# Performance work log

Hardware: AMD Instinct MI355X
Metric: run time of the kernel (lower is better)

## Reference

```python
import jax, jax.numpy as jnp
import numpy as np

DIM = 768
NUM_HEADS = 12
DECAY_RATE = 5.0


def setup_inputs() -> dict:
    key = jax.random.key(0)
    k1, k2, k3, k4 = jax.random.split(key, 4)
    B, N, C = 4, 1024, DIM
    x = jax.random.normal(k1, (B, N, C), dtype=jnp.float32)
    # torch nn.Linear weights: y = x @ W.T ; qkv_bias=False
    qkv_w = jax.random.normal(k2, (3 * C, C), dtype=jnp.float32) * (1.0 / np.sqrt(C))
    proj_w = jax.random.normal(k3, (C, C), dtype=jnp.float32) * (1.0 / np.sqrt(C))
    proj_b = jax.random.normal(k4, (C,), dtype=jnp.float32) * 0.01
    return {"x": x, "qkv_w": qkv_w, "proj_w": proj_w, "proj_b": proj_b, "cur_epoch": 3}


def reference(x, qkv_w, proj_w, proj_b, cur_epoch):
    B, N, C = x.shape
    H = NUM_HEADS
    hd = C // H
    scale = hd ** -0.5

    qkv = (x @ qkv_w.T).reshape(B, N, 3, H, hd).transpose(2, 0, 3, 1, 4)  # [3,B,H,N,hd]
    q, k, v = qkv[0], qkv[1], qkv[2]

    scores = jnp.einsum("bhqd,bhkd->bhqk", q, k) * scale
    logp = jax.nn.log_softmax(scores, axis=-1)
    attn = jnp.exp(logp)  # [B,H,N,N]

    # Per-key entropy: column j of attn flattened over (B,H,N) is renormalized
    # by Categorical; dividing by num_heads cancels under normalization.
    # H(p/s) = log(s) - (1/s) * sum(p * log p)
    s = jnp.sum(attn, axis=(0, 1, 2))                 # [N]
    plogp = jnp.sum(attn * logp, axis=(0, 1, 2))      # [N]
    entropies = jnp.log(s) - plogp / s

    # threshold decay: factor = sum_{i=0}^{cur_epoch-1} decay*exp(-(i+1))
    factor = DECAY_RATE * float(np.sum(np.exp(-(np.arange(cur_epoch) + 1.0))))
    entropy_threshold = float(np.log(C)) - factor

    # attn[:,:,:,keep] @ v[:,:,keep,:] == (attn * mask) @ v  (zeroed columns drop out)
    mask = (entropies <= entropy_threshold).astype(attn.dtype)  # [N]
    out = jnp.einsum("bhqk,bhkd->bhqd", attn * mask[None, None, None, :], v)
    out = out.transpose(0, 2, 1, 3).reshape(B, N, C)
    out = out @ proj_w.T + proj_b
    return out
```

## Files before the change

kernel.cpp:

```cpp
#include <hip/hip_runtime.h>


typedef __bf16 bf16x8 __attribute__((ext_vector_type(8)));
typedef __bf16 bf16x4 __attribute__((ext_vector_type(4)));
typedef float  f32x4  __attribute__((ext_vector_type(4)));

#define MFMA16(a, b, c) __builtin_amdgcn_mfma_f32_16x16x32_bf16((a), (b), (c), 0, 0, 0)
#define LOG2E_8 0.18033688f

__global__ __launch_bounds__(256) void kc_conv(
    const float* __restrict__ x, const float* __restrict__ qw, const float* __restrict__ pw,
    __bf16* __restrict__ xb, __bf16* __restrict__ qwb, __bf16* __restrict__ pwb,
    float* __restrict__ colSP, int* __restrict__ keepCnt)
{
  const int i = blockIdx.x * 256 + threadIdx.x;
  const float4* src;
  __bf16* dst;
  int j;
  if (i < 786432)       { src = (const float4*)x;  dst = xb;  j = i; }
  else if (i < 1228800) { src = (const float4*)qw; dst = qwb; j = i - 786432; }
  else                  { src = (const float4*)pw; dst = pwb; j = i - 1228800; }
  const float4 f = src[j];
  bf16x4 o;
  o[0] = (__bf16)f.x; o[1] = (__bf16)f.y; o[2] = (__bf16)f.z; o[3] = (__bf16)f.w;
  *(bf16x4*)(dst + 4 * (size_t)j) = o;
  if (i < 2048) colSP[i] = 0.f;
  if (i == 0) *keepCnt = 0;
}

__global__ __launch_bounds__(256) void kg_qkv(
    const __bf16* __restrict__ A, const __bf16* __restrict__ Bm,
    __bf16* __restrict__ qb, __bf16* __restrict__ kb, float* __restrict__ v)
{
  __shared__ __bf16 As[2][64 * 72];
  __shared__ __bf16 Bs[2][64 * 72];
  const int tid = threadIdx.x;
  const int w = tid >> 6, lane = tid & 63, quad = lane >> 4, l = lane & 15;
  const int r0 = blockIdx.y * 64, c0 = blockIdx.x * 64;
  const int row = tid >> 3, ko = (tid & 7) * 8;
  const f32x4 zero = {0.f, 0.f, 0.f, 0.f};
  f32x4 acc[4];
#pragma unroll
  for (int ct = 0; ct < 4; ++ct) acc[ct] = zero;

  uint4 a0 = *(const uint4*)(A + (size_t)(r0 + row) * 768 + ko);
  uint4 a1 = *(const uint4*)(A + (size_t)(r0 + row + 32) * 768 + ko);
  uint4 b0 = *(const uint4*)(Bm + (size_t)(c0 + row) * 768 + ko);
  uint4 b1 = *(const uint4*)(Bm + (size_t)(c0 + row + 32) * 768 + ko);

  for (int k0 = 0; k0 < 768; k0 += 64) {
    const int buf = (k0 >> 6) & 1;
    *(uint4*)&As[buf][row * 72 + ko] = a0;
    *(uint4*)&As[buf][(row + 32) * 72 + ko] = a1;
    *(uint4*)&Bs[buf][row * 72 + ko] = b0;
    *(uint4*)&Bs[buf][(row + 32) * 72 + ko] = b1;
    __syncthreads();
    if (k0 < 704) {
      a0 = *(const uint4*)(A + (size_t)(r0 + row) * 768 + k0 + 64 + ko);
      a1 = *(const uint4*)(A + (size_t)(r0 + row + 32) * 768 + k0 + 64 + ko);
      b0 = *(const uint4*)(Bm + (size_t)(c0 + row) * 768 + k0 + 64 + ko);
      b1 = *(const uint4*)(Bm + (size_t)(c0 + row + 32) * 768 + k0 + 64 + ko);
    }
    const bf16x8 af0 = *(const bf16x8*)&As[buf][(w * 16 + l) * 72 + quad * 8];
    const bf16x8 af1 = *(const bf16x8*)&As[buf][(w * 16 + l) * 72 + 32 + quad * 8];
#pragma unroll
    for (int ct = 0; ct < 4; ++ct) {
      const bf16x8 bf0 = *(const bf16x8*)&Bs[buf][(ct * 16 + l) * 72 + quad * 8];
      const bf16x8 bf1 = *(const bf16x8*)&Bs[buf][(ct * 16 + l) * 72 + 32 + quad * 8];
      acc[ct] = MFMA16(af0, bf0, acc[ct]);
      acc[ct] = MFMA16(af1, bf1, acc[ct]);
    }
  }
  const int part = c0 / 768;
  const int h = (c0 % 768) >> 6;
#pragma unroll
  for (int ct = 0; ct < 4; ++ct) {
    const int d = ct * 16 + l;
#pragma unroll
    for (int i = 0; i < 4; ++i) {
      const int rg = r0 + w * 16 + quad * 4 + i;
      const int b_ = rg >> 10, n = rg & 1023;
      const size_t off = ((size_t)(b_ * 12 + h) * 1024 + n) * 64 + d;
      const float val = acc[ct][i];
      if (part == 0)      qb[off] = (__bf16)val;
      else if (part == 1) kb[off] = (__bf16)val;
      else                v[off]  = val;
    }
  }
}

__global__ __launch_bounds__(256) void ks_fused(
    const __bf16* __restrict__ qb, const __bf16* __restrict__ kb,
    float* __restrict__ lse, float* __restrict__ colSP)
{
  __shared__ __bf16 Ks[2][64 * 72];
  __shared__ float sS[1024];
  __shared__ float sP[1024];
  __shared__ float zrow[64];
  const int tid = threadIdx.x;
  const int w = tid >> 6, lane = tid & 63, quad = lane >> 4, l = lane & 15;
  const int bh = blockIdx.x, r0 = blockIdx.y * 64;
  const int row = tid >> 3, ko = (tid & 7) * 8;
  for (int i = tid; i < 1024; i += 256) { sS[i] = 0.f; sP[i] = 0.f; }
  if (tid < 64) zrow[tid] = 0.f;

  const __bf16* qbase = qb + ((size_t)bh * 1024 + r0 + l) * 64;
  bf16x8 aq0[4], aq1[4];
#pragma unroll
  for (int rt = 0; rt < 4; ++rt) {
    aq0[rt] = *(const bf16x8*)(qbase + rt * 1024 + quad * 8);
    aq1[rt] = *(const bf16x8*)(qbase + rt * 1024 + 32 + quad * 8);
  }
  const __bf16* kbase = kb + (size_t)bh * 65536;
  const f32x4 zero = {0.f, 0.f, 0.f, 0.f};
  const int koff = (w * 16 + l) * 72 + quad * 8;

  uint4 ka0 = *(const uint4*)(kbase + (size_t)row * 64 + ko);
  uint4 ka1 = *(const uint4*)(kbase + (size_t)(row + 32) * 64 + ko);

  float z[16] = {};
  for (int s = 0; s < 16; ++s) {
    __bf16* Kw = Ks[s & 1];
    *(uint4*)&Kw[row * 72 + ko] = ka0;
    *(uint4*)&Kw[(row + 32) * 72 + ko] = ka1;
    __syncthreads();
    const int nxt = (s + 1) & 15;
    ka0 = *(const uint4*)(kbase + (size_t)(nxt * 64 + row) * 64 + ko);
    ka1 = *(const uint4*)(kbase + (size_t)(nxt * 64 + row + 32) * 64 + ko);
    const bf16x8 kf0 = *(const bf16x8*)&Kw[koff];
    const bf16x8 kf1 = *(const bf16x8*)&Kw[koff + 32];
#pragma unroll
    for (int rt = 0; rt < 4; ++rt) {
      f32x4 acc = MFMA16(aq0[rt], kf0, zero);
      acc = MFMA16(aq1[rt], kf1, acc);
#pragma unroll
      for (int r = 0; r < 4; ++r) z[rt * 4 + r] += exp2f(acc[r] * LOG2E_8);
    }
  }
#pragma unroll
  for (int off = 1; off < 16; off <<= 1) {
#pragma unroll
    for (int i = 0; i < 16; ++i) z[i] += __shfl_xor(z[i], off);
  }
  if (l == 0) {
#pragma unroll
    for (int rt = 0; rt < 4; ++rt)
#pragma unroll
      for (int r = 0; r < 4; ++r)
        atomicAdd(&zrow[rt * 16 + quad * 4 + r], z[rt * 4 + r]);
  }
  __syncthreads();
  if (tid < 64) lse[bh * 1024 + r0 + tid] = __logf(zrow[tid]);
  float nlb[16], nlg[16];
#pragma unroll
  for (int rt = 0; rt < 4; ++rt) {
#pragma unroll
    for (int r = 0; r < 4; ++r) {
      const float Z = zrow[rt * 16 + quad * 4 + r];
      const float lg = __logf(Z);
      nlg[rt * 4 + r] = -lg;
      nlb[rt * 4 + r] = -lg * 1.44269504f;
    }
  }

  for (int s = 0; s < 16; ++s) {
    __bf16* Kw = Ks[s & 1];
    *(uint4*)&Kw[row * 72 + ko] = ka0;
    *(uint4*)&Kw[(row + 32) * 72 + ko] = ka1;
    __syncthreads();
    if (s < 15) {
      ka0 = *(const uint4*)(kbase + (size_t)((s + 1) * 64 + row) * 64 + ko);
      ka1 = *(const uint4*)(kbase + (size_t)((s + 1) * 64 + row + 32) * 64 + ko);
    }
    const bf16x8 kf0 = *(const bf16x8*)&Kw[koff];
    const bf16x8 kf1 = *(const bf16x8*)&Kw[koff + 32];
    float cs = 0.f, cp = 0.f;
#pragma unroll
    for (int rt = 0; rt < 4; ++rt) {
      f32x4 acc = MFMA16(aq0[rt], kf0, zero);
      acc = MFMA16(aq1[rt], kf1, acc);
#pragma unroll
      for (int r = 0; r < 4; ++r) {
        const float a = acc[r];
        const float t = exp2f(fmaf(a, LOG2E_8, nlb[rt * 4 + r]));
        const float d = fmaf(a, 0.125f, nlg[rt * 4 + r]);
        cs += t;
        cp = fmaf(t, d, cp);
      }
    }
    cs += __shfl_xor(cs, 16); cs += __shfl_xor(cs, 32);
    cp += __shfl_xor(cp, 16); cp += __shfl_xor(cp, 32);
    if (lane < 16) {
      sS[s * 64 + w * 16 + l] += cs;
      sP[s * 64 + w * 16 + l] += cp;
    }
  }
  __syncthreads();
  for (int i = tid; i < 1024; i += 256) {
    atomicAdd(&colSP[i], sS[i]);
    atomicAdd(&colSP[1024 + i], sP[i]);
  }
}

__global__ void k_mask(const float* __restrict__ colSP, const int* __restrict__ cur_epoch,
                       float* __restrict__ mask, int* __restrict__ keepCnt)
{
  const int j = threadIdx.x;
  const float s = colSP[j];
  const float ent = __logf(s) - colSP[1024 + j] / s;
  const int ce = cur_epoch[0];
  float factor = 0.f;
  for (int i = 1; i <= ce; ++i) factor += __expf(-(float)i);
  factor *= 5.0f;
  const float thr = __logf(768.0f) - factor;
  const int keep = (ent <= thr) ? 1 : 0;
  mask[j] = keep ? 1.0f : 0.0f;
  if (keep) atomicAdd(keepCnt, 1);
}

__global__ __launch_bounds__(256) void k_av(
    const __bf16* __restrict__ qb, const __bf16* __restrict__ kb,
    const float* __restrict__ v, const float* __restrict__ lse,
    const float* __restrict__ mask, const int* __restrict__ keepCnt,
    __bf16* __restrict__ ctxb)
{
  if (*keepCnt == 0) return;
  const int tid = threadIdx.x;
  const int bh = blockIdx.x, r0 = blockIdx.y * 32;
  const int b_ = bh / 12, h = bh % 12;
  __shared__ float qs[32][64];
  __shared__ float pbuf[4][8][64];
  for (int i = tid; i < 2048; i += 256)
    qs[i >> 6][i & 63] = (float)qb[((size_t)bh * 1024 + r0) * 64 + i];
  __syncthreads();
  const int w = tid >> 6, l = tid & 63, rb = w * 8;
  float ls[8];
#pragma unroll
  for (int i = 0; i < 8; ++i) ls[i] = lse[bh * 1024 + r0 + rb + i];
  float acc[8] = {};
  for (int chunk = 0; chunk < 16; ++chunk) {
    const float mk = mask[chunk * 64 + l];
    if (__ballot(mk != 0.0f) == 0ull) continue;
    const __bf16* kp = kb + ((size_t)bh * 1024 + chunk * 64 + l) * 64;
    float s[8] = {};
    for (int d0 = 0; d0 < 64; d0 += 8) {
      const bf16x8 kf = *(const bf16x8*)(kp + d0);
#pragma unroll
      for (int dd = 0; dd < 8; ++dd) {
        const float kv = (float)kf[dd];
#pragma unroll
        for (int i = 0; i < 8; ++i) s[i] += qs[rb + i][d0 + dd] * kv;
      }
    }
    __syncthreads();
#pragma unroll
    for (int i = 0; i < 8; ++i)
      pbuf[w][i][l] = __expf(s[i] * 0.125f - ls[i]) * mk;
    __syncthreads();
    const float* vp = v + ((size_t)bh * 1024 + chunk * 64) * 64 + l;
    for (int jj = 0; jj < 64; ++jj) {
      const float vv = vp[(size_t)jj * 64];
#pragma unroll
      for (int i = 0; i < 8; ++i) acc[i] += pbuf[w][i][jj] * vv;
    }
  }
#pragma unroll
  for (int i = 0; i < 8; ++i)
    ctxb[((size_t)(b_ * 1024 + r0 + rb + i)) * 768 + h * 64 + l] = (__bf16)acc[i];
}

__global__ __launch_bounds__(256) void kg_proj(
    const __bf16* __restrict__ A, const __bf16* __restrict__ Bm,
    const float* __restrict__ bias, const int* __restrict__ keepCnt,
    float* __restrict__ out)
{
  const int tid = threadIdx.x;
  const int w = tid >> 6, lane = tid & 63, quad = lane >> 4, l = lane & 15;
  const int r0 = blockIdx.y * 64, c0 = blockIdx.x * 64;
  if (*keepCnt == 0) {
#pragma unroll
    for (int ct = 0; ct < 4; ++ct) {
      const int c = c0 + ct * 16 + l;
      const float bv = bias[c];
#pragma unroll
      for (int i = 0; i < 4; ++i) {
        const int rg = r0 + w * 16 + quad * 4 + i;
        out[(size_t)rg * 768 + c] = bv;
      }
    }
    return;
  }
  __shared__ __bf16 As[64 * 72];
  __shared__ __bf16 Bs[64 * 72];
  const int row = tid >> 3, ko = (tid & 7) * 8;
  const f32x4 zero = {0.f, 0.f, 0.f, 0.f};
  f32x4 acc[4];
#pragma unroll
  for (int ct = 0; ct < 4; ++ct) acc[ct] = zero;

  uint4 a0 = *(const uint4*)(A + (size_t)(r0 + row) * 768 + ko);
  uint4 a1 = *(const uint4*)(A + (size_t)(r0 + row + 32) * 768 + ko);
  uint4 b0 = *(const uint4*)(Bm + (size_t)(c0 + row) * 768 + ko);
  uint4 b1 = *(const uint4*)(Bm + (size_t)(c0 + row + 32) * 768 + ko);

  for (int k0 = 0; k0 < 768; k0 += 64) {
    __syncthreads();
    *(uint4*)&As[row * 72 + ko] = a0;
    *(uint4*)&As[(row + 32) * 72 + ko] = a1;
    *(uint4*)&Bs[row * 72 + ko] = b0;
    *(uint4*)&Bs[(row + 32) * 72 + ko] = b1;
    __syncthreads();
    if (k0 < 704) {
      a0 = *(const uint4*)(A + (size_t)(r0 + row) * 768 + k0 + 64 + ko);
      a1 = *(const uint4*)(A + (size_t)(r0 + row + 32) * 768 + k0 + 64 + ko);
      b0 = *(const uint4*)(Bm + (size_t)(c0 + row) * 768 + k0 + 64 + ko);
      b1 = *(const uint4*)(Bm + (size_t)(c0 + row + 32) * 768 + k0 + 64 + ko);
    }
    const bf16x8 af0 = *(const bf16x8*)&As[(w * 16 + l) * 72 + quad * 8];
    const bf16x8 af1 = *(const bf16x8*)&As[(w * 16 + l) * 72 + 32 + quad * 8];
#pragma unroll
    for (int ct = 0; ct < 4; ++ct) {
      const bf16x8 bf0 = *(const bf16x8*)&Bs[(ct * 16 + l) * 72 + quad * 8];
      const bf16x8 bf1 = *(const bf16x8*)&Bs[(ct * 16 + l) * 72 + 32 + quad * 8];
      acc[ct] = MFMA16(af0, bf0, acc[ct]);
      acc[ct] = MFMA16(af1, bf1, acc[ct]);
    }
  }
#pragma unroll
  for (int ct = 0; ct < 4; ++ct) {
    const int c = c0 + ct * 16 + l;
#pragma unroll
    for (int i = 0; i < 4; ++i) {
      const int rg = r0 + w * 16 + quad * 4 + i;
      out[(size_t)rg * 768 + c] = acc[ct][i] + bias[c];
    }
  }
}

extern "C" void kernel_launch(void* const* d_in, const int* in_sizes, int n_in,
                              void* d_out, int out_size, void* d_ws, size_t ws_size,
                              hipStream_t stream)
{
  const float* x      = (const float*)d_in[0];
  const float* qkv_w  = (const float*)d_in[1];
  const float* proj_w = (const float*)d_in[2];
  const float* proj_b = (const float*)d_in[3];
  const int*   cur_ep = (const int*)d_in[4];

  char* W = (char*)d_ws;
  __bf16* xb    = (__bf16*)(W + 0);
  __bf16* qwb   = (__bf16*)(W + 6291456);
  __bf16* pwb   = (__bf16*)(W + 9830400);
  __bf16* qb    = (__bf16*)(W + 11010048);
  __bf16* kb    = (__bf16*)(W + 17301504);
  float*  v     = (float*) (W + 23592960);
  __bf16* ctxb  = (__bf16*)(W + 36175872);
  float*  lse   = (float*) (W + 42467328);
  float*  mask  = (float*) (W + 42663936);
  int*    keep  = (int*)   (W + 42668032);
  float*  colSP = (float*) (W + 42668544);
  float*  out   = (float*)d_out;

  kc_conv<<<5376, 256, 0, stream>>>(x, qkv_w, proj_w, xb, qwb, pwb, colSP, keep);
  kg_qkv<<<dim3(36, 64), 256, 0, stream>>>(xb, qwb, qb, kb, v);
  ks_fused<<<dim3(48, 16), 256, 0, stream>>>(qb, kb, lse, colSP);
  k_mask<<<1, 1024, 0, stream>>>(colSP, cur_ep, mask, keep);
  k_av<<<dim3(48, 32), 256, 0, stream>>>(qb, kb, v, lse, mask, keep, ctxb);
  kg_proj<<<dim3(12, 64), 256, 0, stream>>>(ctxb, pwb, proj_b, keep, out);
}
```

Baseline: 162.8 us.

## Fuse mask kernel into score kernel via last-block pattern, widen K tile

The separate single-block mask kernel is removed. Its work now runs in ks_fused: the last block to finish, detected through an atomic done counter, computes the per-key entropies and the keep mask. Separately, the K tile per stage doubles from 64 to 128 keys, which halves the number of loop iterations and barriers. This saves one kernel launch and reduces synchronisation overhead, at the cost of more shared memory per block, more registers for the prefetch, and a serial tail in the last block.

```diff
diff --git a/kernel.cpp b/kernel.cpp
--- a/kernel.cpp
+++ b/kernel.cpp
@@ -11,7 +11,7 @@
 __global__ __launch_bounds__(256) void kc_conv(
     const float* __restrict__ x, const float* __restrict__ qw, const float* __restrict__ pw,
     __bf16* __restrict__ xb, __bf16* __restrict__ qwb, __bf16* __restrict__ pwb,
-    float* __restrict__ colSP, int* __restrict__ keepCnt)
+    float* __restrict__ colSP, int* __restrict__ keepCnt, int* __restrict__ doneCnt)
 {
   const int i = blockIdx.x * 256 + threadIdx.x;
   const float4* src;
@@ -25,7 +25,7 @@
   o[0] = (__bf16)f.x; o[1] = (__bf16)f.y; o[2] = (__bf16)f.z; o[3] = (__bf16)f.w;
   *(bf16x4*)(dst + 4 * (size_t)j) = o;
   if (i < 2048) colSP[i] = 0.f;
-  if (i == 0) *keepCnt = 0;
+  if (i == 0) { *keepCnt = 0; *doneCnt = 0; }
 }
 
 __global__ __launch_bounds__(256) void kg_qkv(
@@ -91,12 +91,15 @@
 
 __global__ __launch_bounds__(256) void ks_fused(
     const __bf16* __restrict__ qb, const __bf16* __restrict__ kb,
-    float* __restrict__ lse, float* __restrict__ colSP)
-{
-  __shared__ __bf16 Ks[2][64 * 72];
+    float* __restrict__ lse, float* __restrict__ colSP,
+    const int* __restrict__ cur_epoch, float* __restrict__ mask,
+    int* __restrict__ keepCnt, int* __restrict__ doneCnt)
+{
+  __shared__ __bf16 Ks[2][128 * 72];
   __shared__ float sS[1024];
   __shared__ float sP[1024];
   __shared__ float zrow[64];
+  __shared__ int lastFlag;
   const int tid = threadIdx.x;
   const int w = tid >> 6, lane = tid & 63, quad = lane >> 4, l = lane & 15;
   const int bh = blockIdx.x, r0 = blockIdx.y * 64;
@@ -113,28 +116,35 @@
   }
   const __bf16* kbase = kb + (size_t)bh * 65536;
   const f32x4 zero = {0.f, 0.f, 0.f, 0.f};
-  const int koff = (w * 16 + l) * 72 + quad * 8;
-
-  uint4 ka0 = *(const uint4*)(kbase + (size_t)row * 64 + ko);
-  uint4 ka1 = *(const uint4*)(kbase + (size_t)(row + 32) * 64 + ko);
+
+  uint4 ka[4];
+#pragma unroll
+  for (int t = 0; t < 4; ++t)
+    ka[t] = *(const uint4*)(kbase + (size_t)(t * 32 + row) * 64 + ko);
 
   float z[16] = {};
-  for (int s = 0; s < 16; ++s) {
+  for (int s = 0; s < 8; ++s) {
     __bf16* Kw = Ks[s & 1];
-    *(uint4*)&Kw[row * 72 + ko] = ka0;
-    *(uint4*)&Kw[(row + 32) * 72 + ko] = ka1;
-    __syncthreads();
-    const int nxt = (s + 1) & 15;
-    ka0 = *(const uint4*)(kbase + (size_t)(nxt * 64 + row) * 64 + ko);
-    ka1 = *(const uint4*)(kbase + (size_t)(nxt * 64 + row + 32) * 64 + ko);
-    const bf16x8 kf0 = *(const bf16x8*)&Kw[koff];
-    const bf16x8 kf1 = *(const bf16x8*)&Kw[koff + 32];
-#pragma unroll
-    for (int rt = 0; rt < 4; ++rt) {
-      f32x4 acc = MFMA16(aq0[rt], kf0, zero);
-      acc = MFMA16(aq1[rt], kf1, acc);
-#pragma unroll
-      for (int r = 0; r < 4; ++r) z[rt * 4 + r] += exp2f(acc[r] * LOG2E_8);
+#pragma unroll
+    for (int t = 0; t < 4; ++t)
+      *(uint4*)&Kw[(t * 32 + row) * 72 + ko] = ka[t];
+    __syncthreads();
+    const int nxt = (s + 1) & 7;
+#pragma unroll
+    for (int t = 0; t < 4; ++t)
+      ka[t] = *(const uint4*)(kbase + (size_t)(nxt * 128 + t * 32 + row) * 64 + ko);
+#pragma unroll
+    for (int half = 0; half < 2; ++half) {
+      const int koff = (half * 64 + w * 16 + l) * 72 + quad * 8;
+      const bf16x8 kf0 = *(const bf16x8*)&Kw[koff];
+      const bf16x8 kf1 = *(const bf16x8*)&Kw[koff + 32];
+#pragma unroll
+      for (int rt = 0; rt < 4; ++rt) {
+        f32x4 acc = MFMA16(aq0[rt], kf0, zero);
+        acc = MFMA16(aq1[rt], kf1, acc);
+#pragma unroll
+        for (int r = 0; r < 4; ++r) z[rt * 4 + r] += exp2f(acc[r] * LOG2E_8);
+      }
     }
   }
 #pragma unroll
@@ -163,36 +173,42 @@
     }
   }
 
-  for (int s = 0; s < 16; ++s) {
+  for (int s = 0; s < 8; ++s) {
     __bf16* Kw = Ks[s & 1];
-    *(uint4*)&Kw[row * 72 + ko] = ka0;
-    *(uint4*)&Kw[(row + 32) * 72 + ko] = ka1;
-    __syncthreads();
-    if (s < 15) {
-      ka0 = *(const uint4*)(kbase + (size_t)((s + 1) * 64 + row) * 64 + ko);
-      ka1 = *(const uint4*)(kbase + (size_t)((s + 1) * 64 + row + 32) * 64 + ko);
-    }
-    const bf16x8 kf0 = *(const bf16x8*)&Kw[koff];
-    const bf16x8 kf1 = *(const bf16x8*)&Kw[koff + 32];
-    float cs = 0.f, cp = 0.f;
-#pragma unroll
-    for (int rt = 0; rt < 4; ++rt) {
-      f32x4 acc = MFMA16(aq0[rt], kf0, zero);
-      acc = MFMA16(aq1[rt], kf1, acc);
-#pragma unroll
-      for (int r = 0; r < 4; ++r) {
-        const float a = acc[r];
-        const float t = exp2f(fmaf(a, LOG2E_8, nlb[rt * 4 + r]));
-        const float d = fmaf(a, 0.125f, nlg[rt * 4 + r]);
-        cs += t;
-        cp = fmaf(t, d, cp);
-      }
-    }
-    cs += __shfl_xor(cs, 16); cs += __shfl_xor(cs, 32);
-    cp += __shfl_xor(cp, 16); cp += __shfl_xor(cp, 32);
-    if (lane < 16) {
-      sS[s * 64 + w * 16 + l] += cs;
-      sP[s * 64 + w * 16 + l] += cp;
+#pragma unroll
+    for (int t = 0; t < 4; ++t)
+      *(uint4*)&Kw[(t * 32 + row) * 72 + ko] = ka[t];
+    __syncthreads();
+    if (s < 7) {
+#pragma unroll
+      for (int t = 0; t < 4; ++t)
+        ka[t] = *(const uint4*)(kbase + (size_t)((s + 1) * 128 + t * 32 + row) * 64 + ko);
+    }
+#pragma unroll
+    for (int half = 0; half < 2; ++half) {
+      const int koff = (half * 64 + w * 16 + l) * 72 + quad * 8;
+      const bf16x8 kf0 = *(const bf16x8*)&Kw[koff];
+      const bf16x8 kf1 = *(const bf16x8*)&Kw[koff + 32];
+      float cs = 0.f, cp = 0.f;
+#pragma unroll
+      for (int rt = 0; rt < 4; ++rt) {
+        f32x4 acc = MFMA16(aq0[rt], kf0, zero);
+        acc = MFMA16(aq1[rt], kf1, acc);
+#pragma unroll
+        for (int r = 0; r < 4; ++r) {
+          const float a = acc[r];
+          const float t = exp2f(fmaf(a, LOG2E_8, nlb[rt * 4 + r]));
+          const float d = fmaf(a, 0.125f, nlg[rt * 4 + r]);
+          cs += t;
+          cp = fmaf(t, d, cp);
+        }
+      }
+      cs += __shfl_xor(cs, 16); cs += __shfl_xor(cs, 32);
+      cp += __shfl_xor(cp, 16); cp += __shfl_xor(cp, 32);
+      if (lane < 16) {
+        sS[s * 128 + half * 64 + w * 16 + l] += cs;
+        sP[s * 128 + half * 64 + w * 16 + l] += cp;
+      }
     }
   }
   __syncthreads();
@@ -200,22 +216,32 @@
     atomicAdd(&colSP[i], sS[i]);
     atomicAdd(&colSP[1024 + i], sP[i]);
   }
-}
-
-__global__ void k_mask(const float* __restrict__ colSP, const int* __restrict__ cur_epoch,
-                       float* __restrict__ mask, int* __restrict__ keepCnt)
-{
-  const int j = threadIdx.x;
-  const float s = colSP[j];
-  const float ent = __logf(s) - colSP[1024 + j] / s;
-  const int ce = cur_epoch[0];
-  float factor = 0.f;
-  for (int i = 1; i <= ce; ++i) factor += __expf(-(float)i);
-  factor *= 5.0f;
-  const float thr = __logf(768.0f) - factor;
-  const int keep = (ent <= thr) ? 1 : 0;
-  mask[j] = keep ? 1.0f : 0.0f;
-  if (keep) atomicAdd(keepCnt, 1);
+
+  __threadfence();
+  if (tid == 0) {
+    const int old = atomicAdd(doneCnt, 1);
+    lastFlag = (old == 48 * 16 - 1);
+  }
+  __syncthreads();
+  if (lastFlag) {
+    __threadfence();
+    const int ce = cur_epoch[0];
+    float factor = 0.f;
+    for (int i = 1; i <= ce; ++i) factor += __expf(-(float)i);
+    const float thr = __logf(768.0f) - 5.0f * factor;
+    int kcnt = 0;
+    for (int jj = tid; jj < 1024; jj += 256) {
+      const float sv = atomicAdd(&colSP[jj], 0.0f);
+      const float pv = atomicAdd(&colSP[1024 + jj], 0.0f);
+      const float ent = __logf(sv) - pv / sv;
+      const int kp = (ent <= thr) ? 1 : 0;
+      mask[jj] = kp ? 1.0f : 0.0f;
+      kcnt += kp;
+    }
+#pragma unroll
+    for (int off = 1; off < 64; off <<= 1) kcnt += __shfl_xor(kcnt, off);
+    if ((tid & 63) == 0 && kcnt) atomicAdd(keepCnt, kcnt);
+  }
 }
 
 __global__ __launch_bounds__(256) void k_av(
@@ -359,12 +385,12 @@
   float*  mask  = (float*) (W + 42663936);
   int*    keep  = (int*)   (W + 42668032);
   float*  colSP = (float*) (W + 42668544);
+  int*    done  = (int*)   (W + 42676736);
   float*  out   = (float*)d_out;
 
-  kc_conv<<<5376, 256, 0, stream>>>(x, qkv_w, proj_w, xb, qwb, pwb, colSP, keep);
+  kc_conv<<<5376, 256, 0, stream>>>(x, qkv_w, proj_w, xb, qwb, pwb, colSP, keep, done);
   kg_qkv<<<dim3(36, 64), 256, 0, stream>>>(xb, qwb, qb, kb, v);
-  ks_fused<<<dim3(48, 16), 256, 0, stream>>>(qb, kb, lse, colSP);
-  k_mask<<<1, 1024, 0, stream>>>(colSP, cur_ep, mask, keep);
+  ks_fused<<<dim3(48, 16), 256, 0, stream>>>(qb, kb, lse, colSP, cur_ep, mask, keep, done);
   k_av<<<dim3(48, 32), 256, 0, stream>>>(qb, kb, v, lse, mask, keep, ctxb);
   kg_proj<<<dim3(12, 64), 256, 0, stream>>>(ctxb, pwb, proj_b, keep, out);
 }
```

New measurement: 252.6 us. 1.55x slower.
